# Performance work log

Hardware: AMD Instinct MI355X
Metric: run time of the kernel (lower is better)

Reference implementation:

```python
import jax, jax.numpy as jnp
import numpy as np

BATCH, SEQ, DIM, DSTATE = 8, 2048, 1024, 16


def setup_inputs() -> dict:
    key = jax.random.key(0)
    ks = jax.random.split(key, 8)
    u = jax.random.normal(ks[0], (BATCH, SEQ, DIM), jnp.float32)
    gate = jax.random.normal(ks[1], (BATCH, SEQ, DIM), jnp.float32)
    # parameters (init per module: normal std=0.01 for A_log/B/C, zeros for D)
    A_log = 0.01 * jax.random.normal(ks[2], (DSTATE, DSTATE), jnp.float32)
    B_mat = 0.01 * jax.random.normal(ks[3], (DIM, DSTATE), jnp.float32)
    C_mat = 0.01 * jax.random.normal(ks[4], (DIM, DSTATE), jnp.float32)
    D = jnp.zeros((DIM,), jnp.float32)
    bound = 1.0 / np.sqrt(DIM)  # nn.Linear default init
    dt_w = jax.random.uniform(ks[5], (1, DIM), jnp.float32, -bound, bound)
    dt_b = jax.random.uniform(ks[6], (1,), jnp.float32, -bound, bound)
    return {"u": u, "gate": gate, "A_log": A_log, "B_mat": B_mat,
            "C_mat": C_mat, "D": D, "dt_w": dt_w, "dt_b": dt_b}


def reference(u, gate, A_log, B_mat, C_mat, D, dt_w, dt_b):
    # delta = sigmoid(Linear(gate)) : [B, S, 1] -> [B, S]
    delta = jax.nn.sigmoid(jnp.einsum('bsd,od->bso', gate, dt_w) + dt_b)[..., 0]
    A = -jnp.exp(A_log)                               # [N, N]
    scaled_A = delta[..., None, None] * A             # [B, S, N, N]
    A_exp = jax.scipy.linalg.expm(scaled_A)           # batched matrix exp
    Bu = jnp.einsum('bsd,dn->bsn', u, B_mat)          # [B, S, N]

    def step(h, inp):
        Aexp_t, bu_t = inp                            # [B,N,N], [B,N]
        h = jnp.einsum('bn,bnm->bm', h, Aexp_t) + bu_t
        return h, h

    h0 = jnp.zeros((u.shape[0], DSTATE), u.dtype)
    _, hs = jax.lax.scan(step, h0, (jnp.swapaxes(A_exp, 0, 1), jnp.swapaxes(Bu, 0, 1)))
    hs = jnp.swapaxes(hs, 0, 1)                       # [B, S, N]
    y = jnp.einsum('bsn,dn->bsd', hs, C_mat) + D * u  # [B, S, D]
    return y
```

## Files before the change

### kernel.cpp

```cpp
#include <hip/hip_runtime.h>

#define BATCH  8
#define SEQ    2048
#define DIMSZ  1024
#define NST    16
#define LCH    32
#define CPB    (SEQ / LCH)
#define NCHUNK (BATCH * CPB)
#define NCHEB  32

typedef __attribute__((ext_vector_type(8))) short bf16x8;
typedef __attribute__((ext_vector_type(4))) float f32x4;

static __device__ __forceinline__ unsigned short f2bf(float f) {
    unsigned u = __builtin_bit_cast(unsigned, f);
    unsigned r = (u + 0x7FFFu + ((u >> 16) & 1u)) >> 16;
    return (unsigned short)r;
}
static __device__ __forceinline__ float bf2f(unsigned short h) {
    unsigned u = ((unsigned)h) << 16;
    return __builtin_bit_cast(float, u);
}

__global__ __launch_bounds__(256) void sA_nodes(
    const float* __restrict__ A_log, float* __restrict__ Fn)
{
    __shared__ float Xs[16 * 17];
    __shared__ float Ts[16 * 17];
    const int tid = threadIdx.x;
    const int i = tid >> 4, j = tid & 15;
    const float th = (2.f * blockIdx.x + 1.f) * (3.14159265358979f / 64.f);
    const float dl = 0.5f * (1.f + cosf(th));
    const float a  = -expf(A_log[tid]);
    const float x  = dl * a * (1.0f / 64.0f);
    Xs[i*17 + j] = x;
    Ts[i*17 + j] = x;
    float S = x + (i == j ? 1.0f : 0.0f);
    __syncthreads();
#pragma unroll
    for (int k = 2; k <= 8; ++k) {
        float nt = 0.f;
#pragma unroll
        for (int kk = 0; kk < 16; ++kk)
            nt = fmaf(Ts[i*17 + kk], Xs[kk*17 + j], nt);
        nt *= (1.0f / (float)k);
        S += nt;
        __syncthreads();
        Ts[i*17 + j] = nt;
        __syncthreads();
    }
#pragma unroll
    for (int r = 0; r < 6; ++r) {
        __syncthreads();
        Ts[i*17 + j] = S;
        __syncthreads();
        float nt = 0.f;
#pragma unroll
        for (int kk = 0; kk < 16; ++kk)
            nt = fmaf(Ts[i*17 + kk], Ts[kk*17 + j], nt);
        S = nt;
    }
    Fn[(size_t)blockIdx.x * 256 + tid] = S;
}

__global__ __launch_bounds__(256) void sB_setup(
    const float* __restrict__ Fn, const float* __restrict__ B_mat,
    float* __restrict__ Gt,
    unsigned short* __restrict__ Bfh, unsigned short* __restrict__ Bfl)
{
    const int tid = threadIdx.x;
    const int blk = blockIdx.x;
    if (blk < NCHEB) {
        const int m = blk;
        float acc = 0.f;
        for (int k = 0; k < NCHEB; ++k) {
            const float th = (2.f * k + 1.f) * (3.14159265358979f / 64.f);
            acc = fmaf(Fn[(size_t)k * 256 + tid], cosf(m * th), acc);
        }
        const float sc = (m == 0) ? (1.f / 32.f) : (2.f / 32.f);
        Gt[(size_t)tid * NCHEB + m] = acc * sc;
    } else {
        const int idx0 = (blk - NCHEB) * 2048;
        for (int t = 0; t < 8; ++t) {
            const int idx = idx0 + t * 256 + tid;
            const int j  = idx & 7;
            const int l  = (idx >> 3) & 63;
            const int ks = idx >> 9;
            const int k  = ks * 32 + ((l >> 4) << 3) + j;
            const int n  = l & 15;
            float bv = B_mat[(size_t)k * 16 + n];
            unsigned short h = f2bf(bv);
            Bfh[idx] = h;
            Bfl[idx] = f2bf(bv - bf2f(h));
        }
    }
}

__global__ __launch_bounds__(256) void k1a_delta(
    const float* __restrict__ gate, const float* __restrict__ dt_w,
    const float* __restrict__ dt_b, float* __restrict__ delta)
{
    const int tid  = threadIdx.x;
    const int lane = tid & 63;
    const int w    = tid >> 6;
    const int tok  = blockIdx.x * 4 + w;
    const float* gp = gate + (size_t)tok * DIMSZ;
    float s = 0.f;
#pragma unroll
    for (int i = 0; i < 4; ++i) {
        const float4 g  = *(const float4*)(gp   + i * 256 + lane * 4);
        const float4 wv = *(const float4*)(dt_w + i * 256 + lane * 4);
        s = fmaf(g.x, wv.x, s); s = fmaf(g.y, wv.y, s);
        s = fmaf(g.z, wv.z, s); s = fmaf(g.w, wv.w, s);
    }
#pragma unroll
    for (int off = 32; off >= 1; off >>= 1)
        s += __shfl_xor(s, off, 64);
    if (lane == 0)
        delta[tok] = 1.0f / (1.0f + expf(-(s + dt_b[0])));
}

__global__ __launch_bounds__(256, 2) void kBA(
    const float* __restrict__ u,
    const unsigned short* __restrict__ Bfh, const unsigned short* __restrict__ Bfl,
    const float* __restrict__ Gt, const float* __restrict__ delta,
    float* __restrict__ Bu, float* __restrict__ P, float* __restrict__ e)
{
    __shared__ float smem[8704];
    __shared__ float Bus[LCH * NST];
    __shared__ float dl[LCH];
    __shared__ float sd[1];
    __shared__ float Ps[16 * 17];
    const int tid  = threadIdx.x;
    const int lane = tid & 63;
    const int w    = tid >> 6;
    const size_t gI = blockIdx.x;
    const int tok0 = (int)gI * 32;
    const int half = w & 1;
    const int wrow = (w >> 1) * 16;
    const int q    = lane >> 4;
    const int r    = lane & 15;

    if (tid < LCH) dl[tid] = delta[gI * LCH + tid];

    const uint4* bh = (const uint4*)Bfh;
    const uint4* bl = (const uint4*)Bfl;

    const int srow = 8 * w + (lane >> 5);
    const int p    = lane & 31;
    int colb[4];
#pragma unroll
    for (int i = 0; i < 4; ++i) {
        const int row = srow + 2 * i;
        const int lc  = (p & 16) | ((p & 15) ^ (row & 15));
        colb[i] = ((lc & 16) ? 512 : 0) + (lc & 15) * 4;
    }

    auto stage = [&](int c, int b) {
#pragma unroll
        for (int i = 0; i < 4; ++i) {
            const float* gp = u + (size_t)(tok0 + srow + 2 * i) * DIMSZ
                                + (colb[i] + c * 64);
            __builtin_amdgcn_global_load_lds(
                (const __attribute__((address_space(1))) void*)gp,
                (__attribute__((address_space(3))) void*)&smem[b * 4096 + (8 * w + 2 * i) * 128],
                16, 0, 0);
        }
    };

    f32x4 acc = {0.f, 0.f, 0.f, 0.f};
    uint4 fh[2][2], fl[2][2];

    stage(0, 0);
    stage(1, 1);
    {
        const int ks0 = half * 16;
        fh[0][0] = bh[(ks0 + 0) * 64 + lane]; fl[0][0] = bl[(ks0 + 0) * 64 + lane];
        fh[0][1] = bh[(ks0 + 1) * 64 + lane]; fl[0][1] = bl[(ks0 + 1) * 64 + lane];
    }
    asm volatile("s_waitcnt vmcnt(8)" ::: "memory");
    __builtin_amdgcn_sched_barrier(0);
    __builtin_amdgcn_s_barrier();

#pragma unroll
    for (int c = 0; c < 8; ++c) {
        const int b = c & 1;
        float fu[2][8];
#pragma unroll
        for (int s = 0; s < 2; ++s) {
            const int c16a = (s * 8 + 2 * q + 0) ^ r;
            const int c16b = (s * 8 + 2 * q + 1) ^ r;
            const float4 v0 = *(const float4*)&smem[b * 4096 + (wrow + r) * 128 + (half * 16 + c16a) * 4];
            const float4 v1 = *(const float4*)&smem[b * 4096 + (wrow + r) * 128 + (half * 16 + c16b) * 4];
            fu[s][0] = v0.x; fu[s][1] = v0.y; fu[s][2] = v0.z; fu[s][3] = v0.w;
            fu[s][4] = v1.x; fu[s][5] = v1.y; fu[s][6] = v1.z; fu[s][7] = v1.w;
        }
        asm volatile("s_waitcnt lgkmcnt(0)" ::: "memory");
        __builtin_amdgcn_sched_barrier(0);
        __builtin_amdgcn_s_barrier();
        if (c + 2 < 8) stage(c + 2, b);
        if (c + 1 < 8) {
            const int ks0 = half * 16 + 2 * (c + 1);
            fh[(c + 1) & 1][0] = bh[(ks0 + 0) * 64 + lane];
            fl[(c + 1) & 1][0] = bl[(ks0 + 0) * 64 + lane];
            fh[(c + 1) & 1][1] = bh[(ks0 + 1) * 64 + lane];
            fl[(c + 1) & 1][1] = bl[(ks0 + 1) * 64 + lane];
        }
        __builtin_amdgcn_sched_barrier(0);
#pragma unroll
        for (int s = 0; s < 2; ++s) {
            bf16x8 uh, ul;
#pragma unroll
            for (int i = 0; i < 8; ++i) {
                unsigned short h = f2bf(fu[s][i]);
                uh[i] = (short)h;
                ul[i] = (short)f2bf(fu[s][i] - bf2f(h));
            }
            const bf16x8 Bh = __builtin_bit_cast(bf16x8, fh[b][s]);
            const bf16x8 Bl = __builtin_bit_cast(bf16x8, fl[b][s]);
            acc = __builtin_amdgcn_mfma_f32_16x16x32_bf16(uh, Bh, acc, 0, 0, 0);
            acc = __builtin_amdgcn_mfma_f32_16x16x32_bf16(uh, Bl, acc, 0, 0, 0);
            acc = __builtin_amdgcn_mfma_f32_16x16x32_bf16(ul, Bh, acc, 0, 0, 0);
        }
        if (c < 7) {
            if (c < 6) asm volatile("s_waitcnt vmcnt(8)" ::: "memory");
            else       asm volatile("s_waitcnt vmcnt(4)" ::: "memory");
            __builtin_amdgcn_sched_barrier(0);
            __builtin_amdgcn_s_barrier();
        }
    }

    float* red = smem;
#pragma unroll
    for (int rr = 0; rr < 4; ++rr)
        red[w * 256 + (q * 4 + rr) * 16 + r] = acc[rr];
    __syncthreads();
    const float b0 = red[tid]       + red[256 + tid];
    const float b1 = red[512 + tid] + red[768 + tid];
    Bu[gI * 512 + tid]       = b0;
    Bu[gI * 512 + 256 + tid] = b1;
    Bus[tid]       = b0;
    Bus[256 + tid] = b1;

    float gr[NCHEB];
    {
        const float4* gp = (const float4*)(Gt + (size_t)tid * NCHEB);
#pragma unroll
        for (int qq = 0; qq < NCHEB / 4; ++qq) {
            float4 v = gp[qq];
            gr[qq*4+0] = v.x; gr[qq*4+1] = v.y; gr[qq*4+2] = v.z; gr[qq*4+3] = v.w;
        }
    }
    __syncthreads();
    if (tid == 0) {
        float s = 0.f;
        for (int t = 0; t < LCH; ++t) s += dl[t];
        sd[0] = s;
    }
    for (int t = 0; t < LCH; ++t) {
        const float x = 2.f * dl[t] - 1.f;
        float accm = fmaf(gr[1], x, gr[0]);
        float tm2 = 1.f, tm1 = x;
#pragma unroll
        for (int m = 2; m < NCHEB; ++m) {
            const float tm = fmaf(2.f * x, tm1, -tm2);
            accm = fmaf(gr[m], tm, accm);
            tm2 = tm1; tm1 = tm;
        }
        smem[t * 272 + (tid >> 4) * 17 + (tid & 15)] = accm;
    }
    __syncthreads();
    float S;
    {
        const float xp = 2.f * (sd[0] * (1.f / LCH)) - 1.f;
        float accm = fmaf(gr[1], xp, gr[0]);
        float tm2 = 1.f, tm1 = xp;
#pragma unroll
        for (int m = 2; m < NCHEB; ++m) {
            const float tm = fmaf(2.f * xp, tm1, -tm2);
            accm = fmaf(gr[m], tm, accm);
            tm2 = tm1; tm1 = tm;
        }
        S = accm;
    }
    const int i = tid >> 4, j = tid & 15;
#pragma unroll
    for (int rr = 0; rr < 5; ++rr) {
        Ps[i*17 + j] = S;
        __syncthreads();
        float ns = 0.f;
#pragma unroll
        for (int k = 0; k < 16; ++k)
            ns = fmaf(Ps[i*17 + k], Ps[k*17 + j], ns);
        __syncthreads();
        S = ns;
    }
    P[gI * 256 + tid] = S;
    if (tid < 64) {
        const int gq = tid >> 4, jj = tid & 15, i0 = gq * 4;
        float h = 0.f;
        for (int t = 0; t < LCH; ++t) {
            float pp = 0.f;
#pragma unroll
            for (int m = 0; m < 4; ++m)
                pp = fmaf(__shfl(h, gq * 20 + m, 64),
                          smem[t * 272 + (i0 + m) * 17 + jj], pp);
            pp += __shfl_xor(pp, 16, 64);
            pp += __shfl_xor(pp, 32, 64);
            h = Bus[t * 16 + jj] + pp;
        }
        if (gq == 0) e[gI * NST + jj] = h;
    }
}

__global__ __launch_bounds__(256) void k4_scan(
    const float* __restrict__ P, const float* __restrict__ e,
    float* __restrict__ hin)
{
    __shared__ float Pl[32 * 272];
    __shared__ float el[32 * NST];
    const int tid = threadIdx.x;
    const int b = blockIdx.x;
    float h = 0.f;
    for (int half = 0; half < 2; ++half) {
        const int c0 = half * 32;
        for (int idx = tid; idx < 32*256; idx += 256) {
            const int c = idx >> 8, ij = idx & 255, i = ij >> 4, jj = ij & 15;
            Pl[c*272 + i*17 + jj] = P[((size_t)(b*CPB + c0 + c)) * 256 + ij];
        }
        for (int idx = tid; idx < 32*NST; idx += 256)
            el[idx] = e[((size_t)(b*CPB + c0)) * NST + idx];
        __syncthreads();
        if (tid < 64) {
            const int gq = tid >> 4, j = tid & 15, i0 = gq * 4;
            for (int c = 0; c < 32; ++c) {
                if (tid < 16) hin[((size_t)(b*CPB + c0 + c)) * NST + j] = h;
                float pp = 0.f;
#pragma unroll
                for (int m = 0; m < 4; ++m)
                    pp = fmaf(__shfl(h, gq * 20 + m, 64),
                              Pl[c*272 + (i0 + m)*17 + j], pp);
                pp += __shfl_xor(pp, 16, 64);
                pp += __shfl_xor(pp, 32, 64);
                h = el[c*16 + j] + pp;
            }
        }
        __syncthreads();
    }
}

__global__ __launch_bounds__(256) void k5_out(
    const float* __restrict__ Gt, const float* __restrict__ delta,
    const float* __restrict__ Bu, const float* __restrict__ hin,
    const float* __restrict__ u, const float* __restrict__ C_mat,
    const float* __restrict__ D, float* __restrict__ y)
{
    __shared__ float Mlds[32 * 272];
    __shared__ float Bus[LCH * NST];
    __shared__ float dl[LCH];
    __shared__ __align__(16) float Hs[LCH * NST];
    const int tid = threadIdx.x;
    const size_t g = blockIdx.x;
    if (tid < LCH) dl[tid] = delta[g * LCH + tid];
    for (int idx = tid; idx < LCH * NST; idx += 256)
        Bus[idx] = Bu[g * (size_t)(LCH * NST) + idx];
    float gr[NCHEB];
    {
        const float4* gp = (const float4*)(Gt + (size_t)tid * NCHEB);
#pragma unroll
        for (int qq = 0; qq < NCHEB / 4; ++qq) {
            float4 v = gp[qq];
            gr[qq*4+0] = v.x; gr[qq*4+1] = v.y; gr[qq*4+2] = v.z; gr[qq*4+3] = v.w;
        }
    }
    __syncthreads();
    for (int t = 0; t < LCH; ++t) {
        const float x = 2.f * dl[t] - 1.f;
        float accm = fmaf(gr[1], x, gr[0]);
        float tm2 = 1.f, tm1 = x;
#pragma unroll
        for (int m = 2; m < NCHEB; ++m) {
            const float tm = fmaf(2.f * x, tm1, -tm2);
            accm = fmaf(gr[m], tm, accm);
            tm2 = tm1; tm1 = tm;
        }
        Mlds[t * 272 + (tid >> 4) * 17 + (tid & 15)] = accm;
    }
    __syncthreads();
    if (tid < 64) {
        const int gq = tid >> 4, jj = tid & 15, i0 = gq * 4;
        float h = hin[g * NST + jj];
        for (int t = 0; t < LCH; ++t) {
            float pp = 0.f;
#pragma unroll
            for (int m = 0; m < 4; ++m)
                pp = fmaf(__shfl(h, gq * 20 + m, 64),
                          Mlds[t * 272 + (i0 + m) * 17 + jj], pp);
            pp += __shfl_xor(pp, 16, 64);
            pp += __shfl_xor(pp, 32, 64);
            h = Bus[t * 16 + jj] + pp;
            if (gq == 0) Hs[t * 16 + jj] = h;
        }
    }
    __syncthreads();
    const int d0 = tid * 4;
    float4 cr[4][4];
#pragma unroll
    for (int r = 0; r < 4; ++r)
#pragma unroll
        for (int qq = 0; qq < 4; ++qq)
            cr[r][qq] = ((const float4*)C_mat)[(d0 + r) * 4 + qq];
    const float4 dv = ((const float4*)D)[tid];
    const bool dnz = (dv.x != 0.f) || (dv.y != 0.f) || (dv.z != 0.f) || (dv.w != 0.f);
    for (int t = 0; t < LCH; ++t) {
        const size_t row = (g * LCH + t) * DIMSZ;
        float y0 = 0.f, y1 = 0.f, y2 = 0.f, y3 = 0.f;
        if (dnz) {
            const float4 uv = ((const float4*)(u + row))[tid];
            y0 = dv.x * uv.x; y1 = dv.y * uv.y; y2 = dv.z * uv.z; y3 = dv.w * uv.w;
        }
#pragma unroll
        for (int qq = 0; qq < 4; ++qq) {
            const float4 hq = *((const float4*)&Hs[t*16 + qq*4]);
            y0 = fmaf(hq.x, cr[0][qq].x, y0); y0 = fmaf(hq.y, cr[0][qq].y, y0);
            y0 = fmaf(hq.z, cr[0][qq].z, y0); y0 = fmaf(hq.w, cr[0][qq].w, y0);
            y1 = fmaf(hq.x, cr[1][qq].x, y1); y1 = fmaf(hq.y, cr[1][qq].y, y1);
            y1 = fmaf(hq.z, cr[1][qq].z, y1); y1 = fmaf(hq.w, cr[1][qq].w, y1);
            y2 = fmaf(hq.x, cr[2][qq].x, y2); y2 = fmaf(hq.y, cr[2][qq].y, y2);
            y2 = fmaf(hq.z, cr[2][qq].z, y2); y2 = fmaf(hq.w, cr[2][qq].w, y2);
            y3 = fmaf(hq.x, cr[3][qq].x, y3); y3 = fmaf(hq.y, cr[3][qq].y, y3);
            y3 = fmaf(hq.z, cr[3][qq].z, y3); y3 = fmaf(hq.w, cr[3][qq].w, y3);
        }
        float4 ov; ov.x = y0; ov.y = y1; ov.z = y2; ov.w = y3;
        ((float4*)(y + row))[tid] = ov;
    }
}

extern "C" void kernel_launch(void* const* d_in, const int* in_sizes, int n_in,
                              void* d_out, int out_size, void* d_ws, size_t ws_size,
                              hipStream_t stream)
{
    const float* u     = (const float*)d_in[0];
    const float* gate  = (const float*)d_in[1];
    const float* A_log = (const float*)d_in[2];
    const float* B_mat = (const float*)d_in[3];
    const float* C_mat = (const float*)d_in[4];
    const float* D     = (const float*)d_in[5];
    const float* dt_w  = (const float*)d_in[6];
    const float* dt_b  = (const float*)d_in[7];
    float* y = (float*)d_out;

    float* ws = (float*)d_ws;
    size_t o = 0;
    float* Fn    = ws + o; o += 32 * 256;
    float* Gt    = ws + o; o += 256 * NCHEB;
    float* delta = ws + o; o += (size_t)BATCH * SEQ;
    float* Bu    = ws + o; o += (size_t)BATCH * SEQ * NST;
    float* P     = ws + o; o += (size_t)NCHUNK * 256;
    float* e     = ws + o; o += (size_t)NCHUNK * NST;
    float* hin   = ws + o; o += (size_t)NCHUNK * NST;
    unsigned short* Bfh = (unsigned short*)(ws + o); o += 8192;
    unsigned short* Bfl = (unsigned short*)(ws + o); o += 8192;

    sA_nodes<<<NCHEB, 256, 0, stream>>>(A_log, Fn);
    sB_setup<<<NCHEB + 8, 256, 0, stream>>>(Fn, B_mat, Gt, Bfh, Bfl);
    k1a_delta<<<BATCH * SEQ / 4, 256, 0, stream>>>(gate, dt_w, dt_b, delta);
    kBA     <<<NCHUNK, 256, 0, stream>>>(u, Bfh, Bfl, Gt, delta, Bu, P, e);
    k4_scan <<<BATCH,  256, 0, stream>>>(P, e, hin);
    k5_out  <<<NCHUNK, 256, 0, stream>>>(Gt, delta, Bu, hin, u, C_mat, D, y);
}
```

Measured before the change: 242.7 us.

## Fuse matrix-exp setup, Chebyshev fit and delta into one launch

Merges the three setup kernels (node matrix exponentials, Chebyshev coefficient fit with B bf16 split, and delta computation) into a single kernel. Block 0 does all the setup: each wave handles 8 Chebyshev nodes in turn, and the intermediate Fn values stay in shared memory instead of going through global memory. The remaining blocks compute delta. This removes two kernel launches and one global round trip. The cost is that the setup work, previously spread over 32+ blocks, now runs serially in one block and could become the critical path of the fused launch.

```diff
diff --git a/kernel.cpp b/kernel.cpp
--- a/kernel.cpp
+++ b/kernel.cpp
@@ -8,6 +8,7 @@
 #define CPB    (SEQ / LCH)
 #define NCHUNK (BATCH * CPB)
 #define NCHEB  32
+#define PI_F   3.14159265358979f
 
 typedef __attribute__((ext_vector_type(8))) short bf16x8;
 typedef __attribute__((ext_vector_type(4))) float f32x4;
@@ -22,102 +23,136 @@
     return __builtin_bit_cast(float, u);
 }
 
-__global__ __launch_bounds__(256) void sA_nodes(
-    const float* __restrict__ A_log, float* __restrict__ Fn)
-{
-    __shared__ float Xs[16 * 17];
-    __shared__ float Ts[16 * 17];
-    const int tid = threadIdx.x;
-    const int i = tid >> 4, j = tid & 15;
-    const float th = (2.f * blockIdx.x + 1.f) * (3.14159265358979f / 64.f);
-    const float dl = 0.5f * (1.f + cosf(th));
-    const float a  = -expf(A_log[tid]);
-    const float x  = dl * a * (1.0f / 64.0f);
-    Xs[i*17 + j] = x;
-    Ts[i*17 + j] = x;
-    float S = x + (i == j ? 1.0f : 0.0f);
-    __syncthreads();
-#pragma unroll
-    for (int k = 2; k <= 8; ++k) {
-        float nt = 0.f;
-#pragma unroll
-        for (int kk = 0; kk < 16; ++kk)
-            nt = fmaf(Ts[i*17 + kk], Xs[kk*17 + j], nt);
-        nt *= (1.0f / (float)k);
-        S += nt;
-        __syncthreads();
-        Ts[i*17 + j] = nt;
-        __syncthreads();
-    }
-#pragma unroll
-    for (int r = 0; r < 6; ++r) {
-        __syncthreads();
-        Ts[i*17 + j] = S;
-        __syncthreads();
-        float nt = 0.f;
-#pragma unroll
-        for (int kk = 0; kk < 16; ++kk)
-            nt = fmaf(Ts[i*17 + kk], Ts[kk*17 + j], nt);
-        S = nt;
-    }
-    Fn[(size_t)blockIdx.x * 256 + tid] = S;
-}
-
-__global__ __launch_bounds__(256) void sB_setup(
-    const float* __restrict__ Fn, const float* __restrict__ B_mat,
-    float* __restrict__ Gt,
+__global__ __launch_bounds__(256) void k1_setup_delta(
+    const float* __restrict__ gate, const float* __restrict__ dt_w,
+    const float* __restrict__ dt_b, const float* __restrict__ A_log,
+    const float* __restrict__ B_mat,
+    float* __restrict__ delta, float* __restrict__ Gt,
     unsigned short* __restrict__ Bfh, unsigned short* __restrict__ Bfl)
 {
-    const int tid = threadIdx.x;
-    const int blk = blockIdx.x;
-    if (blk < NCHEB) {
-        const int m = blk;
-        float acc = 0.f;
-        for (int k = 0; k < NCHEB; ++k) {
-            const float th = (2.f * k + 1.f) * (3.14159265358979f / 64.f);
-            acc = fmaf(Fn[(size_t)k * 256 + tid], cosf(m * th), acc);
-        }
-        const float sc = (m == 0) ? (1.f / 32.f) : (2.f / 32.f);
-        Gt[(size_t)tid * NCHEB + m] = acc * sc;
-    } else {
-        const int idx0 = (blk - NCHEB) * 2048;
-        for (int t = 0; t < 8; ++t) {
-            const int idx = idx0 + t * 256 + tid;
-            const int j  = idx & 7;
-            const int l  = (idx >> 3) & 63;
-            const int ks = idx >> 9;
-            const int k  = ks * 32 + ((l >> 4) << 3) + j;
-            const int n  = l & 15;
-            float bv = B_mat[(size_t)k * 16 + n];
-            unsigned short h = f2bf(bv);
-            Bfh[idx] = h;
-            Bfl[idx] = f2bf(bv - bf2f(h));
-        }
-    }
-}
-
-__global__ __launch_bounds__(256) void k1a_delta(
-    const float* __restrict__ gate, const float* __restrict__ dt_w,
-    const float* __restrict__ dt_b, float* __restrict__ delta)
-{
+    __shared__ float Fn_l[32 * 256];
+    __shared__ float XT[4][2][272];
+    __shared__ float cosT[32 * 32];
     const int tid  = threadIdx.x;
     const int lane = tid & 63;
     const int w    = tid >> 6;
-    const int tok  = blockIdx.x * 4 + w;
-    const float* gp = gate + (size_t)tok * DIMSZ;
-    float s = 0.f;
-#pragma unroll
-    for (int i = 0; i < 4; ++i) {
-        const float4 g  = *(const float4*)(gp   + i * 256 + lane * 4);
-        const float4 wv = *(const float4*)(dt_w + i * 256 + lane * 4);
-        s = fmaf(g.x, wv.x, s); s = fmaf(g.y, wv.y, s);
-        s = fmaf(g.z, wv.z, s); s = fmaf(g.w, wv.w, s);
-    }
-#pragma unroll
-    for (int off = 32; off >= 1; off >>= 1)
-        s += __shfl_xor(s, off, 64);
-    if (lane == 0)
-        delta[tok] = 1.0f / (1.0f + expf(-(s + dt_b[0])));
+    const int g    = blockIdx.x;
+
+    if (g > 0) {
+        const int tok  = (g - 1) * 4 + w;
+        const float* gp = gate + (size_t)tok * DIMSZ;
+        float s = 0.f;
+#pragma unroll
+        for (int i = 0; i < 4; ++i) {
+            const float4 gv = *(const float4*)(gp   + i * 256 + lane * 4);
+            const float4 wv = *(const float4*)(dt_w + i * 256 + lane * 4);
+            s = fmaf(gv.x, wv.x, s); s = fmaf(gv.y, wv.y, s);
+            s = fmaf(gv.z, wv.z, s); s = fmaf(gv.w, wv.w, s);
+        }
+#pragma unroll
+        for (int off = 32; off >= 1; off >>= 1)
+            s += __shfl_xor(s, off, 64);
+        if (lane == 0)
+            delta[tok] = 1.0f / (1.0f + expf(-(s + dt_b[0])));
+        return;
+    }
+
+    float* Xw = &XT[w][0][0];
+    float* Tw = &XT[w][1][0];
+    const int jb = lane & 15;
+    const int ib = lane >> 4;
+    for (int nn = 0; nn < 8; ++nn) {
+        const int node = w * 8 + nn;
+        const float th = (2.f * node + 1.f) * (PI_F / 64.f);
+        const float dn = 0.5f * (1.f + cosf(th));
+        float S[4];
+#pragma unroll
+        for (int p = 0; p < 4; ++p) {
+            const int e = lane + 64 * p;
+            const int i = ib + 4 * p;
+            const float a = -expf(A_log[e]);
+            const float x = dn * a * (1.0f / 64.0f);
+            Xw[i * 17 + jb] = x;
+            Tw[i * 17 + jb] = x;
+            S[p] = x + (i == jb ? 1.0f : 0.0f);
+        }
+        __syncthreads();
+#pragma unroll
+        for (int k = 2; k <= 8; ++k) {
+            float nt[4];
+#pragma unroll
+            for (int p = 0; p < 4; ++p) {
+                const int i = ib + 4 * p;
+                float acc = 0.f;
+#pragma unroll
+                for (int kk = 0; kk < 16; ++kk)
+                    acc = fmaf(Tw[i * 17 + kk], Xw[kk * 17 + jb], acc);
+                nt[p] = acc * (1.0f / (float)k);
+                S[p] += nt[p];
+            }
+            __syncthreads();
+#pragma unroll
+            for (int p = 0; p < 4; ++p)
+                Tw[(ib + 4 * p) * 17 + jb] = nt[p];
+            __syncthreads();
+        }
+#pragma unroll
+        for (int r = 0; r < 6; ++r) {
+            __syncthreads();
+#pragma unroll
+            for (int p = 0; p < 4; ++p)
+                Tw[(ib + 4 * p) * 17 + jb] = S[p];
+            __syncthreads();
+#pragma unroll
+            for (int p = 0; p < 4; ++p) {
+                const int i = ib + 4 * p;
+                float acc = 0.f;
+#pragma unroll
+                for (int kk = 0; kk < 16; ++kk)
+                    acc = fmaf(Tw[i * 17 + kk], Tw[kk * 17 + jb], acc);
+                S[p] = acc;
+            }
+        }
+#pragma unroll
+        for (int p = 0; p < 4; ++p)
+            Fn_l[node * 256 + lane + 64 * p] = S[p];
+    }
+#pragma unroll
+    for (int p = 0; p < 4; ++p) {
+        const int idx = tid * 4 + p;
+        const int m = idx >> 5, k = idx & 31;
+        const float th = (2.f * k + 1.f) * (PI_F / 64.f);
+        cosT[idx] = cosf((float)m * th);
+    }
+    __syncthreads();
+    {
+        float acc[NCHEB];
+#pragma unroll
+        for (int m = 0; m < NCHEB; ++m) acc[m] = 0.f;
+        for (int k = 0; k < NCHEB; ++k) {
+            const float f = Fn_l[k * 256 + tid];
+#pragma unroll
+            for (int m = 0; m < NCHEB; ++m)
+                acc[m] = fmaf(f, cosT[m * 32 + k], acc[m]);
+        }
+#pragma unroll
+        for (int m = 0; m < NCHEB; ++m) {
+            const float sc = (m == 0) ? (1.f / 32.f) : (2.f / 32.f);
+            Gt[(size_t)tid * NCHEB + m] = acc[m] * sc;
+        }
+    }
+    for (int t = 0; t < 64; ++t) {
+        const int idx = t * 256 + tid;
+        const int j  = idx & 7;
+        const int l  = (idx >> 3) & 63;
+        const int ks = idx >> 9;
+        const int k  = ks * 32 + ((l >> 4) << 3) + j;
+        const int n  = l & 15;
+        float bv = B_mat[(size_t)k * 16 + n];
+        unsigned short h = f2bf(bv);
+        Bfh[idx] = h;
+        Bfl[idx] = f2bf(bv - bf2f(h));
+    }
 }
 
 __global__ __launch_bounds__(256, 2) void kBA(
@@ -429,7 +464,7 @@
             y2 = fmaf(hq.x, cr[2][qq].x, y2); y2 = fmaf(hq.y, cr[2][qq].y, y2);
             y2 = fmaf(hq.z, cr[2][qq].z, y2); y2 = fmaf(hq.w, cr[2][qq].w, y2);
             y3 = fmaf(hq.x, cr[3][qq].x, y3); y3 = fmaf(hq.y, cr[3][qq].y, y3);
-            y3 = fmaf(hq.z, cr[3][qq].z, y3); y3 = fmaf(hq.w, cr[3][qq].w, y3);
+            y3 = fmaf(hq.w, cr[3][qq].w, y3); y3 = fmaf(hq.z, cr[3][qq].z, y3);
         }
         float4 ov; ov.x = y0; ov.y = y1; ov.z = y2; ov.w = y3;
         ((float4*)(y + row))[tid] = ov;
@@ -452,7 +487,6 @@
 
     float* ws = (float*)d_ws;
     size_t o = 0;
-    float* Fn    = ws + o; o += 32 * 256;
     float* Gt    = ws + o; o += 256 * NCHEB;
     float* delta = ws + o; o += (size_t)BATCH * SEQ;
     float* Bu    = ws + o; o += (size_t)BATCH * SEQ * NST;
@@ -462,10 +496,9 @@
     unsigned short* Bfh = (unsigned short*)(ws + o); o += 8192;
     unsigned short* Bfl = (unsigned short*)(ws + o); o += 8192;
 
-    sA_nodes<<<NCHEB, 256, 0, stream>>>(A_log, Fn);
-    sB_setup<<<NCHEB + 8, 256, 0, stream>>>(Fn, B_mat, Gt, Bfh, Bfl);
-    k1a_delta<<<BATCH * SEQ / 4, 256, 0, stream>>>(gate, dt_w, dt_b, delta);
-    kBA     <<<NCHUNK, 256, 0, stream>>>(u, Bfh, Bfl, Gt, delta, Bu, P, e);
-    k4_scan <<<BATCH,  256, 0, stream>>>(P, e, hin);
-    k5_out  <<<NCHUNK, 256, 0, stream>>>(Gt, delta, Bu, hin, u, C_mat, D, y);
-}
+    k1_setup_delta<<<BATCH * SEQ / 4 + 1, 256, 0, stream>>>(
+        gate, dt_w, dt_b, A_log, B_mat, delta, Gt, Bfh, Bfl);
+    kBA    <<<NCHUNK, 256, 0, stream>>>(u, Bfh, Bfl, Gt, delta, Bu, P, e);
+    k4_scan<<<BATCH,  256, 0, stream>>>(P, e, hin);
+    k5_out <<<NCHUNK, 256, 0, stream>>>(Gt, delta, Bu, hin, u, C_mat, D, y);
+}
```

Result: slower. 286.1 us (+17.9%).

## Double block size in kBA and k5 with triple-buffered u staging

Applied to the files above, without the earlier changes.

Both the Bu/transition kernel and the output kernel now run 512 threads per block instead of 256. In kBA2, eight waves split the K dimension four ways, each handling one MFMA step per stage, and a third LDS buffer deepens the u-load pipeline. In the Chebyshev transition-matrix and output loops, each half of the block now covers 16 of the 32 timesteps. The aim is more latency hiding and per-block parallelism on the 512-block grids, at the cost of larger shared memory, more barriers and a four-way cross-wave reduction.

```diff
diff --git a/kernel.cpp b/kernel.cpp
--- a/kernel.cpp
+++ b/kernel.cpp
@@ -8,6 +8,7 @@
 #define CPB    (SEQ / LCH)
 #define NCHUNK (BATCH * CPB)
 #define NCHEB  32
+#define PI_F   3.14159265358979f
 
 typedef __attribute__((ext_vector_type(8))) short bf16x8;
 typedef __attribute__((ext_vector_type(4))) float f32x4;
@@ -29,7 +30,7 @@
     __shared__ float Ts[16 * 17];
     const int tid = threadIdx.x;
     const int i = tid >> 4, j = tid & 15;
-    const float th = (2.f * blockIdx.x + 1.f) * (3.14159265358979f / 64.f);
+    const float th = (2.f * blockIdx.x + 1.f) * (PI_F / 64.f);
     const float dl = 0.5f * (1.f + cosf(th));
     const float a  = -expf(A_log[tid]);
     const float x  = dl * a * (1.0f / 64.0f);
@@ -74,7 +75,7 @@
         const int m = blk;
         float acc = 0.f;
         for (int k = 0; k < NCHEB; ++k) {
-            const float th = (2.f * k + 1.f) * (3.14159265358979f / 64.f);
+            const float th = (2.f * k + 1.f) * (PI_F / 64.f);
             acc = fmaf(Fn[(size_t)k * 256 + tid], cosf(m * th), acc);
         }
         const float sc = (m == 0) ? (1.f / 32.f) : (2.f / 32.f);
@@ -120,13 +121,13 @@
         delta[tok] = 1.0f / (1.0f + expf(-(s + dt_b[0])));
 }
 
-__global__ __launch_bounds__(256, 2) void kBA(
+__global__ __launch_bounds__(512, 4) void kBA2(
     const float* __restrict__ u,
     const unsigned short* __restrict__ Bfh, const unsigned short* __restrict__ Bfl,
     const float* __restrict__ Gt, const float* __restrict__ delta,
     float* __restrict__ Bu, float* __restrict__ P, float* __restrict__ e)
 {
-    __shared__ float smem[8704];
+    __shared__ float smem[12288];
     __shared__ float Bus[LCH * NST];
     __shared__ float dl[LCH];
     __shared__ float sd[1];
@@ -136,8 +137,8 @@
     const int w    = tid >> 6;
     const size_t gI = blockIdx.x;
     const int tok0 = (int)gI * 32;
-    const int half = w & 1;
-    const int wrow = (w >> 1) * 16;
+    const int qk   = w & 3;
+    const int wrow = (w >> 2) * 16;
     const int q    = lane >> 4;
     const int r    = lane & 15;
 
@@ -146,85 +147,78 @@
     const uint4* bh = (const uint4*)Bfh;
     const uint4* bl = (const uint4*)Bfl;
 
-    const int srow = 8 * w + (lane >> 5);
+    const int srow = 4 * w + (lane >> 5);
     const int p    = lane & 31;
-    int colb[4];
-#pragma unroll
-    for (int i = 0; i < 4; ++i) {
+    int colb[2];
+#pragma unroll
+    for (int i = 0; i < 2; ++i) {
         const int row = srow + 2 * i;
-        const int lc  = (p & 16) | ((p & 15) ^ (row & 15));
-        colb[i] = ((lc & 16) ? 512 : 0) + (lc & 15) * 4;
+        colb[i] = 256 * (p >> 3) + 4 * ((p & 7) ^ (row & 7));
     }
 
     auto stage = [&](int c, int b) {
 #pragma unroll
-        for (int i = 0; i < 4; ++i) {
+        for (int i = 0; i < 2; ++i) {
             const float* gp = u + (size_t)(tok0 + srow + 2 * i) * DIMSZ
-                                + (colb[i] + c * 64);
+                                + (colb[i] + c * 32);
             __builtin_amdgcn_global_load_lds(
                 (const __attribute__((address_space(1))) void*)gp,
-                (__attribute__((address_space(3))) void*)&smem[b * 4096 + (8 * w + 2 * i) * 128],
+                (__attribute__((address_space(3))) void*)&smem[b * 4096 + (4 * w + 2 * i) * 128],
                 16, 0, 0);
         }
     };
 
     f32x4 acc = {0.f, 0.f, 0.f, 0.f};
-    uint4 fh[2][2], fl[2][2];
-
+    uint4 fh[2], fl[2];
+
+    fh[0] = bh[(qk * 8 + 0) * 64 + lane];
+    fl[0] = bl[(qk * 8 + 0) * 64 + lane];
     stage(0, 0);
     stage(1, 1);
-    {
-        const int ks0 = half * 16;
-        fh[0][0] = bh[(ks0 + 0) * 64 + lane]; fl[0][0] = bl[(ks0 + 0) * 64 + lane];
-        fh[0][1] = bh[(ks0 + 1) * 64 + lane]; fl[0][1] = bl[(ks0 + 1) * 64 + lane];
-    }
-    asm volatile("s_waitcnt vmcnt(8)" ::: "memory");
+    stage(2, 2);
+    asm volatile("s_waitcnt vmcnt(4)" ::: "memory");
     __builtin_amdgcn_sched_barrier(0);
     __builtin_amdgcn_s_barrier();
 
 #pragma unroll
     for (int c = 0; c < 8; ++c) {
-        const int b = c & 1;
-        float fu[2][8];
-#pragma unroll
-        for (int s = 0; s < 2; ++s) {
-            const int c16a = (s * 8 + 2 * q + 0) ^ r;
-            const int c16b = (s * 8 + 2 * q + 1) ^ r;
-            const float4 v0 = *(const float4*)&smem[b * 4096 + (wrow + r) * 128 + (half * 16 + c16a) * 4];
-            const float4 v1 = *(const float4*)&smem[b * 4096 + (wrow + r) * 128 + (half * 16 + c16b) * 4];
-            fu[s][0] = v0.x; fu[s][1] = v0.y; fu[s][2] = v0.z; fu[s][3] = v0.w;
-            fu[s][4] = v1.x; fu[s][5] = v1.y; fu[s][6] = v1.z; fu[s][7] = v1.w;
+        const int b = c % 3;
+        float fu[8];
+        {
+            const int c0 = qk * 8 + ((2 * q + 0) ^ (r & 7));
+            const int c1 = qk * 8 + ((2 * q + 1) ^ (r & 7));
+            const float4 v0 = *(const float4*)&smem[b * 4096 + (wrow + r) * 128 + c0 * 4];
+            const float4 v1 = *(const float4*)&smem[b * 4096 + (wrow + r) * 128 + c1 * 4];
+            fu[0] = v0.x; fu[1] = v0.y; fu[2] = v0.z; fu[3] = v0.w;
+            fu[4] = v1.x; fu[5] = v1.y; fu[6] = v1.z; fu[7] = v1.w;
         }
         asm volatile("s_waitcnt lgkmcnt(0)" ::: "memory");
         __builtin_amdgcn_sched_barrier(0);
         __builtin_amdgcn_s_barrier();
-        if (c + 2 < 8) stage(c + 2, b);
         if (c + 1 < 8) {
-            const int ks0 = half * 16 + 2 * (c + 1);
-            fh[(c + 1) & 1][0] = bh[(ks0 + 0) * 64 + lane];
-            fl[(c + 1) & 1][0] = bl[(ks0 + 0) * 64 + lane];
-            fh[(c + 1) & 1][1] = bh[(ks0 + 1) * 64 + lane];
-            fl[(c + 1) & 1][1] = bl[(ks0 + 1) * 64 + lane];
-        }
+            const int ks = qk * 8 + c + 1;
+            fh[(c + 1) & 1] = bh[ks * 64 + lane];
+            fl[(c + 1) & 1] = bl[ks * 64 + lane];
+        }
+        if (c + 3 < 8) stage(c + 3, (c + 3) % 3);
         __builtin_amdgcn_sched_barrier(0);
-#pragma unroll
-        for (int s = 0; s < 2; ++s) {
+        {
             bf16x8 uh, ul;
 #pragma unroll
             for (int i = 0; i < 8; ++i) {
-                unsigned short h = f2bf(fu[s][i]);
+                unsigned short h = f2bf(fu[i]);
                 uh[i] = (short)h;
-                ul[i] = (short)f2bf(fu[s][i] - bf2f(h));
+                ul[i] = (short)f2bf(fu[i] - bf2f(h));
             }
-            const bf16x8 Bh = __builtin_bit_cast(bf16x8, fh[b][s]);
-            const bf16x8 Bl = __builtin_bit_cast(bf16x8, fl[b][s]);
+            const bf16x8 Bh = __builtin_bit_cast(bf16x8, fh[c & 1]);
+            const bf16x8 Bl = __builtin_bit_cast(bf16x8, fl[c & 1]);
             acc = __builtin_amdgcn_mfma_f32_16x16x32_bf16(uh, Bh, acc, 0, 0, 0);
             acc = __builtin_amdgcn_mfma_f32_16x16x32_bf16(uh, Bl, acc, 0, 0, 0);
             acc = __builtin_amdgcn_mfma_f32_16x16x32_bf16(ul, Bh, acc, 0, 0, 0);
         }
         if (c < 7) {
-            if (c < 6) asm volatile("s_waitcnt vmcnt(8)" ::: "memory");
-            else       asm volatile("s_waitcnt vmcnt(4)" ::: "memory");
+            if (c == 6) asm volatile("s_waitcnt vmcnt(4)" ::: "memory");
+            else        asm volatile("s_waitcnt vmcnt(6)" ::: "memory");
             __builtin_amdgcn_sched_barrier(0);
             __builtin_amdgcn_s_barrier();
         }
@@ -235,16 +229,16 @@
     for (int rr = 0; rr < 4; ++rr)
         red[w * 256 + (q * 4 + rr) * 16 + r] = acc[rr];
     __syncthreads();
-    const float b0 = red[tid]       + red[256 + tid];
-    const float b1 = red[512 + tid] + red[768 + tid];
-    Bu[gI * 512 + tid]       = b0;
-    Bu[gI * 512 + 256 + tid] = b1;
-    Bus[tid]       = b0;
-    Bus[256 + tid] = b1;
-
+    float bv;
+    if (tid < 256) bv = red[tid]       + red[256 + tid] + red[512 + tid]  + red[768 + tid];
+    else           bv = red[768 + tid] + red[1024 + tid] + red[1280 + tid] + red[1536 + tid];
+    Bu[gI * 512 + tid] = bv;
+    Bus[tid] = bv;
+
+    const int el = tid & 255;
     float gr[NCHEB];
     {
-        const float4* gp = (const float4*)(Gt + (size_t)tid * NCHEB);
+        const float4* gp = (const float4*)(Gt + (size_t)el * NCHEB);
 #pragma unroll
         for (int qq = 0; qq < NCHEB / 4; ++qq) {
             float4 v = gp[qq];
@@ -257,7 +251,8 @@
         for (int t = 0; t < LCH; ++t) s += dl[t];
         sd[0] = s;
     }
-    for (int t = 0; t < LCH; ++t) {
+    const int tgrp = tid >> 8;
+    for (int t = tgrp * 16; t < tgrp * 16 + 16; ++t) {
         const float x = 2.f * dl[t] - 1.f;
         float accm = fmaf(gr[1], x, gr[0]);
         float tm2 = 1.f, tm1 = x;
@@ -267,7 +262,7 @@
             accm = fmaf(gr[m], tm, accm);
             tm2 = tm1; tm1 = tm;
         }
-        smem[t * 272 + (tid >> 4) * 17 + (tid & 15)] = accm;
+        smem[t * 272 + (el >> 4) * 17 + (el & 15)] = accm;
     }
     __syncthreads();
     float S;
@@ -283,10 +278,10 @@
         }
         S = accm;
     }
-    const int i = tid >> 4, j = tid & 15;
+    const int i = el >> 4, j = el & 15;
 #pragma unroll
     for (int rr = 0; rr < 5; ++rr) {
-        Ps[i*17 + j] = S;
+        if (tid < 256) Ps[i*17 + j] = S;
         __syncthreads();
         float ns = 0.f;
 #pragma unroll
@@ -295,7 +290,7 @@
         __syncthreads();
         S = ns;
     }
-    P[gI * 256 + tid] = S;
+    if (tid < 256) P[gI * 256 + tid] = S;
     if (tid < 64) {
         const int gq = tid >> 4, jj = tid & 15, i0 = gq * 4;
         float h = 0.f;
@@ -349,7 +344,7 @@
     }
 }
 
-__global__ __launch_bounds__(256) void k5_out(
+__global__ __launch_bounds__(512, 4) void k5b(
     const float* __restrict__ Gt, const float* __restrict__ delta,
     const float* __restrict__ Bu, const float* __restrict__ hin,
     const float* __restrict__ u, const float* __restrict__ C_mat,
@@ -361,12 +356,13 @@
     __shared__ __align__(16) float Hs[LCH * NST];
     const int tid = threadIdx.x;
     const size_t g = blockIdx.x;
+    const int el = tid & 255;
+    const int tgrp = tid >> 8;
     if (tid < LCH) dl[tid] = delta[g * LCH + tid];
-    for (int idx = tid; idx < LCH * NST; idx += 256)
-        Bus[idx] = Bu[g * (size_t)(LCH * NST) + idx];
+    Bus[tid] = Bu[g * 512 + tid];
     float gr[NCHEB];
     {
-        const float4* gp = (const float4*)(Gt + (size_t)tid * NCHEB);
+        const float4* gp = (const float4*)(Gt + (size_t)el * NCHEB);
 #pragma unroll
         for (int qq = 0; qq < NCHEB / 4; ++qq) {
             float4 v = gp[qq];
@@ -374,7 +370,7 @@
         }
     }
     __syncthreads();
-    for (int t = 0; t < LCH; ++t) {
+    for (int t = tgrp * 16; t < tgrp * 16 + 16; ++t) {
         const float x = 2.f * dl[t] - 1.f;
         float accm = fmaf(gr[1], x, gr[0]);
         float tm2 = 1.f, tm1 = x;
@@ -384,7 +380,7 @@
             accm = fmaf(gr[m], tm, accm);
             tm2 = tm1; tm1 = tm;
         }
-        Mlds[t * 272 + (tid >> 4) * 17 + (tid & 15)] = accm;
+        Mlds[t * 272 + (el >> 4) * 17 + (el & 15)] = accm;
     }
     __syncthreads();
     if (tid < 64) {
@@ -403,20 +399,20 @@
         }
     }
     __syncthreads();
-    const int d0 = tid * 4;
+    const int d0 = el * 4;
     float4 cr[4][4];
 #pragma unroll
     for (int r = 0; r < 4; ++r)
 #pragma unroll
         for (int qq = 0; qq < 4; ++qq)
             cr[r][qq] = ((const float4*)C_mat)[(d0 + r) * 4 + qq];
-    const float4 dv = ((const float4*)D)[tid];
+    const float4 dv = ((const float4*)D)[el];
     const bool dnz = (dv.x != 0.f) || (dv.y != 0.f) || (dv.z != 0.f) || (dv.w != 0.f);
-    for (int t = 0; t < LCH; ++t) {
+    for (int t = tgrp * 16; t < tgrp * 16 + 16; ++t) {
         const size_t row = (g * LCH + t) * DIMSZ;
         float y0 = 0.f, y1 = 0.f, y2 = 0.f, y3 = 0.f;
         if (dnz) {
-            const float4 uv = ((const float4*)(u + row))[tid];
+            const float4 uv = ((const float4*)(u + row))[el];
             y0 = dv.x * uv.x; y1 = dv.y * uv.y; y2 = dv.z * uv.z; y3 = dv.w * uv.w;
         }
 #pragma unroll
@@ -432,7 +428,7 @@
             y3 = fmaf(hq.z, cr[3][qq].z, y3); y3 = fmaf(hq.w, cr[3][qq].w, y3);
         }
         float4 ov; ov.x = y0; ov.y = y1; ov.z = y2; ov.w = y3;
-        ((float4*)(y + row))[tid] = ov;
+        ((float4*)(y + row))[el] = ov;
     }
 }
 
@@ -462,10 +458,10 @@
     unsigned short* Bfh = (unsigned short*)(ws + o); o += 8192;
     unsigned short* Bfl = (unsigned short*)(ws + o); o += 8192;
 
-    sA_nodes<<<NCHEB, 256, 0, stream>>>(A_log, Fn);
-    sB_setup<<<NCHEB + 8, 256, 0, stream>>>(Fn, B_mat, Gt, Bfh, Bfl);
+    sA_nodes <<<NCHEB,     256, 0, stream>>>(A_log, Fn);
+    sB_setup <<<NCHEB + 8, 256, 0, stream>>>(Fn, B_mat, Gt, Bfh, Bfl);
     k1a_delta<<<BATCH * SEQ / 4, 256, 0, stream>>>(gate, dt_w, dt_b, delta);
-    kBA     <<<NCHUNK, 256, 0, stream>>>(u, Bfh, Bfl, Gt, delta, Bu, P, e);
-    k4_scan <<<BATCH,  256, 0, stream>>>(P, e, hin);
-    k5_out  <<<NCHUNK, 256, 0, stream>>>(Gt, delta, Bu, hin, u, C_mat, D, y);
-}
+    kBA2     <<<NCHUNK,    512, 0, stream>>>(u, Bfh, Bfl, Gt, delta, Bu, P, e);
+    k4_scan  <<<BATCH,     256, 0, stream>>>(P, e, hin);
+    k5b      <<<NCHUNK,    512, 0, stream>>>(Gt, delta, Bu, hin, u, C_mat, D, y);
+}
```

Measured after the change: 249.3 us. 2.7% more time.
